# Performance work log

Hardware: AMD Instinct MI355X
Metric: run time of the kernel (lower is better)

## Reference

```python
import jax, jax.numpy as jnp
import numpy as np

N_WIRES = 10
N_LAYERS = 4


def _cnot(state, c, t):
    # state: (2,)*N_WIRES per-sample state tensor; CNOT(control=c, target=t)
    s0 = jnp.take(state, 0, axis=c)
    s1 = jnp.take(state, 1, axis=c)
    tt = t if t < c else t - 1  # target axis index after removing control axis
    s1 = jnp.flip(s1, axis=tt)  # X on target where control == 1
    return jnp.stack([s0, s1], axis=c)


def _circuit(x, params):
    # x: (N_WIRES,) angles. RY(x_i) on |0> -> [cos(x_i/2), sin(x_i/2)] product state.
    q = jnp.stack([jnp.cos(x / 2), jnp.sin(x / 2)], axis=-1).astype(jnp.complex64)  # (n, 2)
    state = q[0]
    for i in range(1, N_WIRES):
        state = jnp.tensordot(state, q[i], axes=0)  # -> (2,)*N_WIRES
    half = jnp.array([-0.5, 0.5], dtype=jnp.float32)
    for layer in range(N_LAYERS):
        # RZ(params[layer, i]) on each wire: diagonal phase exp(-i*theta/2), exp(+i*theta/2)
        for i in range(N_WIRES):
            ph = jnp.exp(1j * (half * params[layer, i]))  # (2,) complex64
            shape = [1] * N_WIRES
            shape[i] = 2
            state = state * ph.reshape(shape)
        # CNOT ladder 0->1, 1->2, ..., (n-2)->(n-1), then (n-1)->0
        for i in range(N_WIRES - 1):
            state = _cnot(state, i, i + 1)
        state = _cnot(state, N_WIRES - 1, 0)
    return state.reshape(-1)  # (2**N_WIRES,)


def _states(X, params):
    return jax.vmap(lambda x: _circuit(x, params))(X)  # (B, 2**N_WIRES) complex64


def setup_inputs() -> dict:
    key = jax.random.key(0)
    k1, k2, k3 = jax.random.split(key, 3)
    two_pi = 2.0 * np.pi
    X = jax.random.uniform(k1, (4096, N_WIRES), jnp.float32, 0.0, two_pi)
    Y = jax.random.uniform(k2, (4096, N_WIRES), jnp.float32, 0.0, two_pi)
    params = jax.random.normal(k3, (N_LAYERS, N_WIRES), dtype=jnp.float32)
    return {"X": X, "Y": Y, "params": params}


def reference(X, Y, params):
    sX = _states(X, params)                 # (Nx, D) complex64
    sY = _states(Y, params)                 # (Ny, D) complex64
    M = sX @ sY.conj().T                    # (Nx, Ny) complex overlaps
    return M.real ** 2 + M.imag ** 2        # |<psi_x|psi_y>|^2
```

## Files before the change

kernel.cpp:

```cpp
#include <hip/hip_runtime.h>


#define NS 4096
#define NW 10

__global__ __launch_bounds__(256) void qkm_precompute(
    const float* __restrict__ X, const float* __restrict__ Y,
    float2* __restrict__ csx, float2* __restrict__ csy) {
    int tid = blockIdx.x * 256 + threadIdx.x;
    int set = tid / (NW * NS);
    int rem = tid - set * (NW * NS);
    int w = rem >> 12;
    int sample = rem & (NS - 1);
    const float* src = set ? Y : X;
    float2* dst = set ? csy : csx;
    float a = 0.5f * src[sample * NW + w];
    float s, c;
    sincosf(a, &s, &c);
    dst[w * NS + sample] = make_float2(c, s);
}

__global__ __launch_bounds__(256) void qkm_gram(
    const float2* __restrict__ csx, const float2* __restrict__ csy,
    float* __restrict__ out) {
    const int col = (blockIdx.x * 256 + threadIdx.x) * 4;
    const int row0 = blockIdx.y * 8;

    float yc[NW][4], ys[NW][4];
#pragma unroll
    for (int w = 0; w < NW; ++w) {
        const float4* p = reinterpret_cast<const float4*>(csy + w * NS + col);
        float4 a = p[0];
        float4 b = p[1];
        yc[w][0] = a.x; ys[w][0] = a.y;
        yc[w][1] = a.z; ys[w][1] = a.w;
        yc[w][2] = b.x; ys[w][2] = b.y;
        yc[w][3] = b.z; ys[w][3] = b.w;
    }

#pragma unroll 2
    for (int r = 0; r < 8; ++r) {
        const int row = row0 + r;
        float p0 = 1.f, p1 = 1.f, p2 = 1.f, p3 = 1.f;
#pragma unroll
        for (int w = 0; w < NW; ++w) {
            const float2 xc = csx[w * NS + row];
            p0 *= fmaf(xc.y, ys[w][0], xc.x * yc[w][0]);
            p1 *= fmaf(xc.y, ys[w][1], xc.x * yc[w][1]);
            p2 *= fmaf(xc.y, ys[w][2], xc.x * yc[w][2]);
            p3 *= fmaf(xc.y, ys[w][3], xc.x * yc[w][3]);
        }
        float4 o;
        o.x = p0 * p0; o.y = p1 * p1; o.z = p2 * p2; o.w = p3 * p3;
        *reinterpret_cast<float4*>(out + (size_t)row * NS + col) = o;
    }
}

extern "C" void kernel_launch(void* const* d_in, const int* in_sizes, int n_in,
                              void* d_out, int out_size, void* d_ws, size_t ws_size,
                              hipStream_t stream) {
    const float* X = (const float*)d_in[0];
    const float* Y = (const float*)d_in[1];
    float* out = (float*)d_out;

    float2* csx = (float2*)d_ws;
    float2* csy = csx + NW * NS;

    qkm_precompute<<<(2 * NW * NS) / 256, 256, 0, stream>>>(X, Y, csx, csy);

    dim3 grid(NS / (256 * 4), NS / 8);
    qkm_gram<<<grid, 256, 0, stream>>>(csx, csy, out);
}
```

Baseline: 100.8 us.

## Fuse sincos precompute into gram kernel with shared-memory X rows

New measurement: 225.8 us. +124.0%, slower.

```diff
diff --git a/kernel.cpp b/kernel.cpp
--- a/kernel.cpp
+++ b/kernel.cpp
@@ -3,56 +3,53 @@
 
 #define NS 4096
 #define NW 10
+#define ROWS 16
 
-__global__ __launch_bounds__(256) void qkm_precompute(
+__global__ __launch_bounds__(256, 4) void qkm_fused(
     const float* __restrict__ X, const float* __restrict__ Y,
-    float2* __restrict__ csx, float2* __restrict__ csy) {
-    int tid = blockIdx.x * 256 + threadIdx.x;
-    int set = tid / (NW * NS);
-    int rem = tid - set * (NW * NS);
-    int w = rem >> 12;
-    int sample = rem & (NS - 1);
-    const float* src = set ? Y : X;
-    float2* dst = set ? csy : csx;
-    float a = 0.5f * src[sample * NW + w];
-    float s, c;
-    sincosf(a, &s, &c);
-    dst[w * NS + sample] = make_float2(c, s);
-}
+    float* __restrict__ out) {
+    __shared__ float2 xcs[ROWS][NW];
 
-__global__ __launch_bounds__(256) void qkm_gram(
-    const float2* __restrict__ csx, const float2* __restrict__ csy,
-    float* __restrict__ out) {
-    const int col = (blockIdx.x * 256 + threadIdx.x) * 4;
-    const int row0 = blockIdx.y * 8;
+    const int col  = (blockIdx.x * 256 + threadIdx.x) * 4;
+    const int row0 = blockIdx.y * ROWS;
+
+    if (threadIdx.x < ROWS * NW) {
+        int r = threadIdx.x / NW;
+        int w = threadIdx.x - r * NW;
+        float s, c;
+        __sincosf(0.5f * X[(row0 + r) * NW + w], &s, &c);
+        xcs[r][w] = make_float2(c, s);
+    }
 
     float yc[NW][4], ys[NW][4];
 #pragma unroll
-    for (int w = 0; w < NW; ++w) {
-        const float4* p = reinterpret_cast<const float4*>(csy + w * NS + col);
-        float4 a = p[0];
-        float4 b = p[1];
-        yc[w][0] = a.x; ys[w][0] = a.y;
-        yc[w][1] = a.z; ys[w][1] = a.w;
-        yc[w][2] = b.x; ys[w][2] = b.y;
-        yc[w][3] = b.z; ys[w][3] = b.w;
+    for (int j = 0; j < 4; ++j) {
+        const float* yp = Y + (size_t)(col + j) * NW;
+#pragma unroll
+        for (int w = 0; w < NW; ++w) {
+            float s, c;
+            __sincosf(0.5f * yp[w], &s, &c);
+            yc[w][j] = c;
+            ys[w][j] = s;
+        }
     }
 
-#pragma unroll 2
-    for (int r = 0; r < 8; ++r) {
-        const int row = row0 + r;
+    __syncthreads();
+
+#pragma unroll 4
+    for (int r = 0; r < ROWS; ++r) {
         float p0 = 1.f, p1 = 1.f, p2 = 1.f, p3 = 1.f;
 #pragma unroll
         for (int w = 0; w < NW; ++w) {
-            const float2 xc = csx[w * NS + row];
-            p0 *= fmaf(xc.y, ys[w][0], xc.x * yc[w][0]);
-            p1 *= fmaf(xc.y, ys[w][1], xc.x * yc[w][1]);
-            p2 *= fmaf(xc.y, ys[w][2], xc.x * yc[w][2]);
-            p3 *= fmaf(xc.y, ys[w][3], xc.x * yc[w][3]);
+            const float2 x = xcs[r][w];
+            p0 *= fmaf(x.y, ys[w][0], x.x * yc[w][0]);
+            p1 *= fmaf(x.y, ys[w][1], x.x * yc[w][1]);
+            p2 *= fmaf(x.y, ys[w][2], x.x * yc[w][2]);
+            p3 *= fmaf(x.y, ys[w][3], x.x * yc[w][3]);
         }
         float4 o;
         o.x = p0 * p0; o.y = p1 * p1; o.z = p2 * p2; o.w = p3 * p3;
-        *reinterpret_cast<float4*>(out + (size_t)row * NS + col) = o;
+        *reinterpret_cast<float4*>(out + (size_t)(row0 + r) * NS + col) = o;
     }
 }
 
@@ -63,11 +60,6 @@
     const float* Y = (const float*)d_in[1];
     float* out = (float*)d_out;
 
-    float2* csx = (float2*)d_ws;
-    float2* csy = csx + NW * NS;
-
-    qkm_precompute<<<(2 * NW * NS) / 256, 256, 0, stream>>>(X, Y, csx, csy);
-
-    dim3 grid(NS / (256 * 4), NS / 8);
-    qkm_gram<<<grid, 256, 0, stream>>>(csx, csy, out);
+    dim3 grid(NS / (256 * 4), NS / ROWS);
+    qkm_fused<<<grid, 256, 0, stream>>>(X, Y, out);
 }
```
